# Optimization experiments

Hardware: AMD Instinct MI355X
Metric: run time of the kernel (lower is better)

Reference implementation:

```python
import jax, jax.numpy as jnp
import numpy as np

HIDDEN = 256

def setup_inputs() -> dict:
    key = jax.random.key(0)
    ks = jax.random.split(key, 7)
    B, S, H = 4, 4096, HIDDEN
    x = jax.random.normal(ks[0], (B, S, H), dtype=jnp.float32)
    s = 1.0 / np.sqrt(H)
    Wq = jax.random.normal(ks[1], (H, H), dtype=jnp.float32) * s
    bq = jax.random.normal(ks[2], (H,), dtype=jnp.float32) * s
    Wk = jax.random.normal(ks[3], (H, H), dtype=jnp.float32) * s
    bk = jax.random.normal(ks[4], (H,), dtype=jnp.float32) * s
    Wv = jax.random.normal(ks[5], (H, H), dtype=jnp.float32) * s
    bv = jax.random.normal(ks[6], (H,), dtype=jnp.float32) * s
    return {"x": x, "Wq": Wq, "bq": bq, "Wk": Wk, "bk": bk, "Wv": Wv, "bv": bv}

def reference(x, Wq, bq, Wk, bk, Wv, bv):
    # Linear projections (torch Linear: x @ W.T + b; here W stored as [in,out])
    Q = x @ Wq + bq  # [B,S,H]
    K = x @ Wk + bk
    V = x @ Wv + bv
    S = x.shape[1]
    # NOTE: original module has NO 1/sqrt(d) scaling — kept faithful.
    scores = jnp.einsum('bqh,bkh->bqk', Q, K)  # [B,S,S]
    causal = jnp.tril(jnp.ones((S, S), dtype=bool))
    scores = jnp.where(causal, scores, -jnp.inf)
    attn = jax.nn.softmax(scores, axis=-1)
    return jnp.einsum('bqk,bkh->bqh', attn, V)
```

## Files before the change

### kernel.cpp

```cpp
#include <hip/hip_runtime.h>
#include <stdint.h>

#define HD   256
#define SEQ  4096
#define NB   4
#define NROW (NB * SEQ)
#define SLOTS_PER_BATCH 144

typedef __attribute__((ext_vector_type(8))) short short8;
typedef __attribute__((ext_vector_type(4))) float f32x4;
typedef __attribute__((ext_vector_type(16))) float f32x16;
typedef _Float16 v8h __attribute__((ext_vector_type(8)));

__device__ __forceinline__ unsigned short f2bf(float f) {
  union { float f; unsigned u; } v; v.f = f;
  unsigned u = v.u;
  u += 0x7fffu + ((u >> 16) & 1u);
  return (unsigned short)(u >> 16);
}
__device__ __forceinline__ float bf2f(unsigned short h) {
  union { float f; unsigned u; } v; v.u = ((unsigned)h) << 16;
  return v.f;
}
__device__ __forceinline__ unsigned short f2h(float f) {
  union { _Float16 h; unsigned short u; } v;
  v.h = (_Float16)f;
  return v.u;
}

__device__ __forceinline__ f32x4 mfma16(short8 a, short8 b, f32x4 c) {
  return __builtin_amdgcn_mfma_f32_16x16x32_bf16(a, b, c, 0, 0, 0);
}
__device__ __forceinline__ f32x16 mfma32h(v8h a, v8h b, f32x16 c) {
  return __builtin_amdgcn_mfma_f32_32x32x16_f16(a, b, c, 0, 0, 0);
}

__device__ __forceinline__ void gload_lds16(const void* g, void* l) {
  __builtin_amdgcn_global_load_lds((const __attribute__((address_space(1))) void*)g,
                                   (__attribute__((address_space(3))) void*)l,
                                   16, 0, 0);
}

__device__ __forceinline__ unsigned pk2h(float a, float b) {
  return (unsigned)f2h(a) | ((unsigned)f2h(b) << 16);
}

__global__ __launch_bounds__(256) void prep_x_kernel(
    const float* __restrict__ x,
    unsigned short* __restrict__ xh, unsigned short* __restrict__ xl)
{
  int i = blockIdx.x * 256 + threadIdx.x;
  const float* p = x + i * 8;
  f32x4 a0 = *(const f32x4*)p;
  f32x4 a1 = *(const f32x4*)(p + 4);
  short8 hh, ll;
#pragma unroll
  for (int j = 0; j < 4; ++j) {
    unsigned short h0 = f2bf(a0[j]);
    hh[j]     = (short)h0;
    ll[j]     = (short)f2bf(a0[j] - bf2f(h0));
    unsigned short h1 = f2bf(a1[j]);
    hh[4 + j] = (short)h1;
    ll[4 + j] = (short)f2bf(a1[j] - bf2f(h1));
  }
  *(short8*)(xh + i * 8) = hh;
  *(short8*)(xl + i * 8) = ll;
}

__global__ __launch_bounds__(256) void prep_w_kernel(
    const float* __restrict__ Wq, const float* __restrict__ Wk,
    const float* __restrict__ Wv,
    unsigned short* __restrict__ WTh, unsigned short* __restrict__ WTl)
{
  int flat = blockIdx.x * 256 + threadIdx.x;
  int mat = flat >> 16;
  int e   = flat & 65535;
  int o   = e >> 8;
  int k   = e & 255;
  const float* W = (mat == 0) ? Wq : (mat == 1) ? Wk : Wv;
  float v = W[k * 256 + o];
  unsigned short h = f2bf(v);
  WTh[flat] = h;
  WTl[flat] = f2bf(v - bf2f(h));
}

__global__ __launch_bounds__(256) void proj_kernel(
    const unsigned short* __restrict__ xh, const unsigned short* __restrict__ xl,
    const unsigned short* __restrict__ WTh, const unsigned short* __restrict__ WTl,
    const float* __restrict__ bq, const float* __restrict__ bk,
    const float* __restrict__ bv,
    unsigned short* __restrict__ Qf, unsigned short* __restrict__ Kf,
    unsigned short* __restrict__ VT)
{
  const int mat = blockIdx.y;
  const int r0  = blockIdx.x << 6;
  const int tid = threadIdx.x;
  const int w    = tid >> 6;
  const int lane = tid & 63;
  const int lr   = lane & 15;
  const int hi4  = lane >> 4;
  const int r4   = hi4 << 2;

  const unsigned short* wth = WTh + (mat << 16);
  const unsigned short* wtl = WTl + (mat << 16);

  f32x4 acc[4][4] = {};

#pragma unroll
  for (int ks = 0; ks < 8; ++ks) {
    short8 ah[4], al[4];
#pragma unroll
    for (int m = 0; m < 4; ++m) {
      int off = (r0 + (m << 4) + lr) * 256 + (ks << 5) + (hi4 << 3);
      ah[m] = *(const short8*)(xh + off);
      al[m] = *(const short8*)(xl + off);
    }
#pragma unroll
    for (int n = 0; n < 4; ++n) {
      int o = (w << 6) + (n << 4) + lr;
      short8 bh = *(const short8*)(wth + o * 256 + (ks << 5) + (hi4 << 3));
      short8 bl = *(const short8*)(wtl + o * 256 + (ks << 5) + (hi4 << 3));
#pragma unroll
      for (int m = 0; m < 4; ++m) acc[m][n] = mfma16(ah[m], bh, acc[m][n]);
#pragma unroll
      for (int m = 0; m < 4; ++m) acc[m][n] = mfma16(al[m], bh, acc[m][n]);
#pragma unroll
      for (int m = 0; m < 4; ++m) acc[m][n] = mfma16(ah[m], bl, acc[m][n]);
    }
  }

  const float* bias = (mat == 0) ? bq : (mat == 1) ? bk : bv;
#pragma unroll
  for (int n = 0; n < 4; ++n) {
    int col = (w << 6) + (n << 4) + lr;
    float bb = bias[col];
#pragma unroll
    for (int m = 0; m < 4; ++m) {
#pragma unroll
      for (int reg = 0; reg < 4; ++reg) {
        int row = r0 + (m << 4) + r4 + reg;
        float val = acc[m][n][reg] + bb;
        unsigned short h = f2h(val);
        if (mat == 0) {
          Qf[row * 256 + col] = h;
        } else if (mat == 1) {
          Kf[row * 256 + col] = h;
        } else {
          int b = row >> 12, s = row & 4095;
          VT[(b << 20) + (col << 12) + s] = h;
        }
      }
    }
  }
}

__global__ __launch_bounds__(256, 2) void attn_kernel(
    const unsigned short* __restrict__ Qf, const unsigned short* __restrict__ Kf,
    const unsigned short* __restrict__ VT,
    unsigned short* __restrict__ Opart, float* __restrict__ Mpart,
    float* __restrict__ Lpart)
{
  __shared__ __align__(16) unsigned short sK[64 * 256];
  __shared__ __align__(16) unsigned short sV[256 * 64];

  const int bx    = blockIdx.x;
  const int batch = bx & 3;
  const int rk    = bx >> 2;
  int j = 0, pj = 0;
  while (rk >= pj + ((j + 4) >> 2)) { pj += (j + 4) >> 2; ++j; }
  const int c   = rk - pj;
  const int kt0 = c << 3;
  const int kt1 = min(kt0 + 8, 2 * j + 2);
  const int slot = batch * SLOTS_PER_BATCH + pj + c;

  const int tid  = threadIdx.x;
  const int w    = tid >> 6;
  const int lane = tid & 63;
  const int lc   = lane & 31;
  const int hi   = lane >> 5;

  const unsigned short* Kf_b = Kf + (batch << 20);
  const unsigned short* VT_b = VT + (batch << 20);

  auto stage = [&](int kt) {
#pragma unroll
    for (int it = 0; it < 8; ++it) {
      int id = it * 256 + tid;
      int kr = id >> 5, cb = id & 31;
      gload_lds16(Kf_b + (((kt << 6) + kr) << 8) + (((cb ^ kr) & 31) << 3),
                  sK + id * 8);
      int hd = id >> 3, cb2 = id & 7;
      gload_lds16(VT_b + (hd << 12) + (kt << 6) + (((cb2 ^ (hd >> 2)) & 7) << 3),
                  sV + id * 8);
    }
  };

  f32x16 oacc[8];
  float m_ = -1e30f, accl = 0.f;
#pragma unroll
  for (int n = 0; n < 8; ++n)
#pragma unroll
    for (int r = 0; r < 16; ++r) oacc[n][r] = 0.f;

  for (int kt = kt0; kt < kt1; ++kt) {
    stage(kt);
    __syncthreads();

    int qrow = (batch << 12) + (j << 7) + (w << 5) + lc;
    uintptr_t qv = (uintptr_t)Qf + ((size_t)qrow << 9) + (hi << 4);
    asm volatile("" : "+v"(qv));
    const unsigned short* qp = (const unsigned short*)qv;

    f32x16 s0, s1;
#pragma unroll
    for (int r = 0; r < 16; ++r) { s0[r] = 0.f; s1[r] = 0.f; }
    __builtin_amdgcn_s_setprio(1);
#pragma unroll
    for (int ks = 0; ks < 16; ++ks) {
      int cc = (ks << 1) + hi;
      v8h qa  = *(const v8h*)(qp + (ks << 4));
      v8h kb0 = *(const v8h*)(sK + (lc << 8) + (((cc ^ lc) & 31) << 3));
      v8h kb1 = *(const v8h*)(sK + ((32 + lc) << 8) + (((cc ^ lc) & 31) << 3));
      s0 = mfma32h(kb0, qa, s0);
      s1 = mfma32h(kb1, qa, s1);
    }
    __builtin_amdgcn_s_setprio(0);

    const int qg = (j << 7) + (w << 5) + lc;
    if ((kt << 6) + 63 > (j << 7) + (w << 5)) {
#pragma unroll
      for (int r = 0; r < 16; ++r) {
        int kl = (kt << 6) + (r & 3) + ((r >> 2) << 3) + (hi << 2);
        if (kl > qg)      s0[r] = -3e38f;
        if (kl + 32 > qg) s1[r] = -3e38f;
      }
    }

    float mx = fmaxf(s0[0], s1[0]);
#pragma unroll
    for (int r = 1; r < 16; ++r) mx = fmaxf(mx, fmaxf(s0[r], s1[r]));
    mx = fmaxf(mx, __shfl_xor(mx, 32));

    if (__any(mx > m_ + 8.0f)) {
      float mn = fmaxf(m_, mx);
      float sc = __expf(m_ - mn);
      m_ = mn;
      accl *= sc;
#pragma unroll
      for (int r = 0; r < 16; ++r) {
        float scr = __shfl(sc, (r & 3) + ((r >> 2) << 3) + (hi << 2));
#pragma unroll
        for (int n = 0; n < 8; ++n) oacc[n][r] *= scr;
      }
    }

#pragma unroll
    for (int r = 0; r < 16; ++r) {
      s0[r] = __expf(s0[r] - m_);
      s1[r] = __expf(s1[r] - m_);
      accl += s0[r] + s1[r];
    }

    v8h pa[4];
#pragma unroll
    for (int half = 0; half < 2; ++half) {
      const f32x16& ps = half ? s1 : s0;
#pragma unroll
      for (int t2 = 0; t2 < 2; ++t2) {
        int b = t2 << 3;
        unsigned X0 = pk2h(ps[b + 0], ps[b + 1]);
        unsigned X1 = pk2h(ps[b + 2], ps[b + 3]);
        unsigned Y0 = pk2h(ps[b + 4], ps[b + 5]);
        unsigned Y1 = pk2h(ps[b + 6], ps[b + 7]);
        unsigned xs0 = (unsigned)__shfl_xor((int)X0, 32);
        unsigned xs1 = (unsigned)__shfl_xor((int)X1, 32);
        unsigned ys0 = (unsigned)__shfl_xor((int)Y0, 32);
        unsigned ys1 = (unsigned)__shfl_xor((int)Y1, 32);
        union { unsigned u[4]; v8h h; } pu;
        pu.u[0] = hi ? ys0 : X0;
        pu.u[1] = hi ? ys1 : X1;
        pu.u[2] = hi ? Y0 : xs0;
        pu.u[3] = hi ? Y1 : xs1;
        pa[(half << 1) + t2] = pu.h;
      }
    }

    __builtin_amdgcn_s_setprio(1);
#pragma unroll
    for (int ks2 = 0; ks2 < 4; ++ks2) {
      int cc = (ks2 << 1) + hi;
#pragma unroll
      for (int n = 0; n < 8; ++n) {
        int hd = (n << 5) + lc;
        v8h vb = *(const v8h*)(sV + (hd << 6) + (((cc ^ (hd >> 2)) & 7) << 3));
        oacc[n] = mfma32h(pa[ks2], vb, oacc[n]);
      }
    }
    __builtin_amdgcn_s_setprio(0);

    __syncthreads();
  }

  {
    unsigned short* Op = Opart + (size_t)slot * (128 * 256);
    float lt  = accl + __shfl_xor(accl, 32);
    float inv = (lt > 0.f) ? (1.0f / lt) : 0.f;
#pragma unroll
    for (int n = 0; n < 8; ++n) {
#pragma unroll
      for (int r = 0; r < 16; ++r) {
        int crow = (r & 3) + ((r >> 2) << 3) + (hi << 2);
        float invr = __shfl(inv, crow);
        Op[((w << 5) + crow) * 256 + (n << 5) + lc] = f2h(oacc[n][r] * invr);
      }
    }
    if (lane < 32) {
      Mpart[slot * 128 + (w << 5) + lc] = m_;
      Lpart[slot * 128 + (w << 5) + lc] = lt;
    }
  }
}

__global__ __launch_bounds__(256) void merge_kernel(
    const unsigned short* __restrict__ Opart, const float* __restrict__ Mpart,
    const float* __restrict__ Lpart, float* __restrict__ out)
{
  int t = blockIdx.x * 256 + threadIdx.x;
  int row = t >> 5, c8 = t & 31;
  int batch = row >> 12, wi = row & 4095;
  int j = wi >> 7, rloc = wi & 127;
  int q  = j >> 2;
  int pj = 2 * q * (q + 1) + (j - 4 * q) * (q + 1);
  int nch = (j + 4) >> 2;
  int sbase = batch * SLOTS_PER_BATCH + pj;

  float M = -1e30f;
  for (int i = 0; i < nch; ++i)
    M = fmaxf(M, Mpart[(sbase + i) * 128 + rloc]);

  float denom = 0.f;
  float r8[8] = {0.f, 0.f, 0.f, 0.f, 0.f, 0.f, 0.f, 0.f};
  for (int i = 0; i < nch; ++i) {
    float mi = Mpart[(sbase + i) * 128 + rloc];
    float li = Lpart[(sbase + i) * 128 + rloc];
    float wgt = __expf(mi - M) * li;
    denom += wgt;
    const unsigned short* Op =
        Opart + ((size_t)(sbase + i) * 128 + rloc) * 256 + (c8 << 3);
    v8h v = *(const v8h*)Op;
#pragma unroll
    for (int qq = 0; qq < 8; ++qq) r8[qq] += wgt * (float)v[qq];
  }
  float inv = 1.0f / denom;
  float* op = out + (size_t)row * 256 + (c8 << 3);
  f32x4 r0, r1;
#pragma unroll
  for (int qq = 0; qq < 4; ++qq) { r0[qq] = r8[qq] * inv; r1[qq] = r8[4 + qq] * inv; }
  *(f32x4*)op = r0;
  *(f32x4*)(op + 4) = r1;
}

extern "C" void kernel_launch(void* const* d_in, const int* in_sizes, int n_in,
                              void* d_out, int out_size, void* d_ws, size_t ws_size,
                              hipStream_t stream) {
  (void)in_sizes; (void)n_in; (void)out_size; (void)ws_size;
  const float* x  = (const float*)d_in[0];
  const float* Wq = (const float*)d_in[1];
  const float* bq = (const float*)d_in[2];
  const float* Wk = (const float*)d_in[3];
  const float* bk = (const float*)d_in[4];
  const float* Wv = (const float*)d_in[5];
  const float* bv = (const float*)d_in[6];
  float* out = (float*)d_out;

  const int nslots = NB * SLOTS_PER_BATCH;
  unsigned short* Qf = (unsigned short*)d_ws;
  unsigned short* Kf = Qf + (size_t)NROW * HD;
  unsigned short* VT = Kf + (size_t)NROW * HD;
  float* Mpart = (float*)(VT + (size_t)NROW * HD);
  float* Lpart = Mpart + (size_t)nslots * 128;
  unsigned short* regionBase = (unsigned short*)(Lpart + (size_t)nslots * 128);
  unsigned short* xh  = regionBase;
  unsigned short* xl  = xh + (size_t)NROW * HD;
  unsigned short* WTh = xl + (size_t)NROW * HD;
  unsigned short* WTl = WTh + 3 * 65536;
  unsigned short* Opart = regionBase;

  hipLaunchKernelGGL(prep_x_kernel, dim3(2048), dim3(256), 0, stream,
                     x, xh, xl);
  hipLaunchKernelGGL(prep_w_kernel, dim3(768), dim3(256), 0, stream,
                     Wq, Wk, Wv, WTh, WTl);
  hipLaunchKernelGGL(proj_kernel, dim3(256, 3), dim3(256), 0, stream,
                     xh, xl, WTh, WTl, bq, bk, bv, Qf, Kf, VT);
  hipLaunchKernelGGL(attn_kernel, dim3(NB * SLOTS_PER_BATCH), dim3(256), 0, stream,
                     Qf, Kf, VT, Opart, Mpart, Lpart);
  hipLaunchKernelGGL(merge_kernel, dim3(2048), dim3(256), 0, stream,
                     Opart, Mpart, Lpart, out);
}
```

Baseline: 233.7 us.

## Fuse x bf16 split into projection and double-buffer 32-key attention tiles

Removes the separate prep_x kernel and its xh/xl workspace by converting fp32 x to hi/lo bf16 inside the projection kernel's operand loads. The attention kernel now uses 32-key tiles with two LDS buffers, issuing the next tile's global-to-LDS loads before computing the current one and waiting with vmcnt plus raw barriers instead of syncthreads. This aims to hide K/V load latency and save a kernel launch plus an x round trip. In exchange there are more loop iterations with smaller MFMA batches, more softmax rescale checks, and the conversion is recomputed three times (once per projection matrix).

```diff
diff --git a/kernel.cpp b/kernel.cpp
--- a/kernel.cpp
+++ b/kernel.cpp
@@ -43,28 +43,6 @@
 
 __device__ __forceinline__ unsigned pk2h(float a, float b) {
   return (unsigned)f2h(a) | ((unsigned)f2h(b) << 16);
-}
-
-__global__ __launch_bounds__(256) void prep_x_kernel(
-    const float* __restrict__ x,
-    unsigned short* __restrict__ xh, unsigned short* __restrict__ xl)
-{
-  int i = blockIdx.x * 256 + threadIdx.x;
-  const float* p = x + i * 8;
-  f32x4 a0 = *(const f32x4*)p;
-  f32x4 a1 = *(const f32x4*)(p + 4);
-  short8 hh, ll;
-#pragma unroll
-  for (int j = 0; j < 4; ++j) {
-    unsigned short h0 = f2bf(a0[j]);
-    hh[j]     = (short)h0;
-    ll[j]     = (short)f2bf(a0[j] - bf2f(h0));
-    unsigned short h1 = f2bf(a1[j]);
-    hh[4 + j] = (short)h1;
-    ll[4 + j] = (short)f2bf(a1[j] - bf2f(h1));
-  }
-  *(short8*)(xh + i * 8) = hh;
-  *(short8*)(xl + i * 8) = ll;
 }
 
 __global__ __launch_bounds__(256) void prep_w_kernel(
@@ -85,7 +63,7 @@
 }
 
 __global__ __launch_bounds__(256) void proj_kernel(
-    const unsigned short* __restrict__ xh, const unsigned short* __restrict__ xl,
+    const float* __restrict__ x,
     const unsigned short* __restrict__ WTh, const unsigned short* __restrict__ WTl,
     const float* __restrict__ bq, const float* __restrict__ bk,
     const float* __restrict__ bv,
@@ -111,9 +89,20 @@
     short8 ah[4], al[4];
 #pragma unroll
     for (int m = 0; m < 4; ++m) {
-      int off = (r0 + (m << 4) + lr) * 256 + (ks << 5) + (hi4 << 3);
-      ah[m] = *(const short8*)(xh + off);
-      al[m] = *(const short8*)(xl + off);
+      const float* xp = x + (r0 + (m << 4) + lr) * 256 + (ks << 5) + (hi4 << 3);
+      f32x4 a0 = *(const f32x4*)xp;
+      f32x4 a1 = *(const f32x4*)(xp + 4);
+      short8 hh, ll;
+#pragma unroll
+      for (int jj = 0; jj < 4; ++jj) {
+        unsigned short h0 = f2bf(a0[jj]);
+        hh[jj]     = (short)h0;
+        ll[jj]     = (short)f2bf(a0[jj] - bf2f(h0));
+        unsigned short h1 = f2bf(a1[jj]);
+        hh[4 + jj] = (short)h1;
+        ll[4 + jj] = (short)f2bf(a1[jj] - bf2f(h1));
+      }
+      ah[m] = hh; al[m] = ll;
     }
 #pragma unroll
     for (int n = 0; n < 4; ++n) {
@@ -160,8 +149,8 @@
     unsigned short* __restrict__ Opart, float* __restrict__ Mpart,
     float* __restrict__ Lpart)
 {
-  __shared__ __align__(16) unsigned short sK[64 * 256];
-  __shared__ __align__(16) unsigned short sV[256 * 64];
+  __shared__ __align__(16) unsigned short sK[2][32 * 256];
+  __shared__ __align__(16) unsigned short sV[2][256 * 32];
 
   const int bx    = blockIdx.x;
   const int batch = bx & 3;
@@ -169,8 +158,8 @@
   int j = 0, pj = 0;
   while (rk >= pj + ((j + 4) >> 2)) { pj += (j + 4) >> 2; ++j; }
   const int c   = rk - pj;
-  const int kt0 = c << 3;
-  const int kt1 = min(kt0 + 8, 2 * j + 2);
+  const int kt0 = c << 4;
+  const int kt1 = min(kt0 + 16, 4 * j + 4);
   const int slot = batch * SLOTS_PER_BATCH + pj + c;
 
   const int tid  = threadIdx.x;
@@ -182,16 +171,16 @@
   const unsigned short* Kf_b = Kf + (batch << 20);
   const unsigned short* VT_b = VT + (batch << 20);
 
-  auto stage = [&](int kt) {
-#pragma unroll
-    for (int it = 0; it < 8; ++it) {
+  auto stage = [&](int kt, int buf) {
+#pragma unroll
+    for (int it = 0; it < 4; ++it) {
       int id = it * 256 + tid;
       int kr = id >> 5, cb = id & 31;
-      gload_lds16(Kf_b + (((kt << 6) + kr) << 8) + (((cb ^ kr) & 31) << 3),
-                  sK + id * 8);
-      int hd = id >> 3, cb2 = id & 7;
-      gload_lds16(VT_b + (hd << 12) + (kt << 6) + (((cb2 ^ (hd >> 2)) & 7) << 3),
-                  sV + id * 8);
+      gload_lds16(Kf_b + (((kt << 5) + kr) << 8) + (((cb ^ kr) & 31) << 3),
+                  &sK[buf][id * 8]);
+      int hd = id >> 2, cb2 = id & 3;
+      gload_lds16(VT_b + (hd << 12) + (kt << 5) + (((cb2 ^ (hd >> 2)) & 3) << 3),
+                  &sV[buf][id * 8]);
     }
   };
 
@@ -202,43 +191,50 @@
 #pragma unroll
     for (int r = 0; r < 16; ++r) oacc[n][r] = 0.f;
 
+  const int qg = (j << 7) + (w << 5) + lc;
+
+  stage(kt0, 0);
+  int cur = 0;
+
   for (int kt = kt0; kt < kt1; ++kt) {
-    stage(kt);
-    __syncthreads();
-
-    int qrow = (batch << 12) + (j << 7) + (w << 5) + lc;
+    const bool havenext = (kt + 1 < kt1);
+    if (havenext) stage(kt + 1, cur ^ 1);
+    __builtin_amdgcn_sched_barrier(0);
+    if (havenext) { asm volatile("s_waitcnt vmcnt(8)" ::: "memory"); }
+    else          { asm volatile("s_waitcnt vmcnt(0)" ::: "memory"); }
+    __builtin_amdgcn_sched_barrier(0);
+    __builtin_amdgcn_s_barrier();
+    __builtin_amdgcn_sched_barrier(0);
+
+    int qrow = (batch << 12) + qg;
     uintptr_t qv = (uintptr_t)Qf + ((size_t)qrow << 9) + (hi << 4);
     asm volatile("" : "+v"(qv));
     const unsigned short* qp = (const unsigned short*)qv;
 
-    f32x16 s0, s1;
-#pragma unroll
-    for (int r = 0; r < 16; ++r) { s0[r] = 0.f; s1[r] = 0.f; }
+    f32x16 s0;
+#pragma unroll
+    for (int r = 0; r < 16; ++r) s0[r] = 0.f;
     __builtin_amdgcn_s_setprio(1);
 #pragma unroll
     for (int ks = 0; ks < 16; ++ks) {
       int cc = (ks << 1) + hi;
       v8h qa  = *(const v8h*)(qp + (ks << 4));
-      v8h kb0 = *(const v8h*)(sK + (lc << 8) + (((cc ^ lc) & 31) << 3));
-      v8h kb1 = *(const v8h*)(sK + ((32 + lc) << 8) + (((cc ^ lc) & 31) << 3));
+      v8h kb0 = *(const v8h*)(&sK[cur][(lc << 8) + (((cc ^ lc) & 31) << 3)]);
       s0 = mfma32h(kb0, qa, s0);
-      s1 = mfma32h(kb1, qa, s1);
     }
     __builtin_amdgcn_s_setprio(0);
 
-    const int qg = (j << 7) + (w << 5) + lc;
-    if ((kt << 6) + 63 > (j << 7) + (w << 5)) {
+    if ((kt << 5) + 31 > (j << 7) + (w << 5)) {
 #pragma unroll
       for (int r = 0; r < 16; ++r) {
-        int kl = (kt << 6) + (r & 3) + ((r >> 2) << 3) + (hi << 2);
-        if (kl > qg)      s0[r] = -3e38f;
-        if (kl + 32 > qg) s1[r] = -3e38f;
-      }
-    }
-
-    float mx = fmaxf(s0[0], s1[0]);
-#pragma unroll
-    for (int r = 1; r < 16; ++r) mx = fmaxf(mx, fmaxf(s0[r], s1[r]));
+        int kl = (kt << 5) + (r & 3) + ((r >> 2) << 3) + (hi << 2);
+        if (kl > qg) s0[r] = -3e38f;
+      }
+    }
+
+    float mx = s0[0];
+#pragma unroll
+    for (int r = 1; r < 16; ++r) mx = fmaxf(mx, s0[r]);
     mx = fmaxf(mx, __shfl_xor(mx, 32));
 
     if (__any(mx > m_ + 8.0f)) {
@@ -257,48 +253,46 @@
 #pragma unroll
     for (int r = 0; r < 16; ++r) {
       s0[r] = __expf(s0[r] - m_);
-      s1[r] = __expf(s1[r] - m_);
-      accl += s0[r] + s1[r];
-    }
-
-    v8h pa[4];
-#pragma unroll
-    for (int half = 0; half < 2; ++half) {
-      const f32x16& ps = half ? s1 : s0;
-#pragma unroll
-      for (int t2 = 0; t2 < 2; ++t2) {
-        int b = t2 << 3;
-        unsigned X0 = pk2h(ps[b + 0], ps[b + 1]);
-        unsigned X1 = pk2h(ps[b + 2], ps[b + 3]);
-        unsigned Y0 = pk2h(ps[b + 4], ps[b + 5]);
-        unsigned Y1 = pk2h(ps[b + 6], ps[b + 7]);
-        unsigned xs0 = (unsigned)__shfl_xor((int)X0, 32);
-        unsigned xs1 = (unsigned)__shfl_xor((int)X1, 32);
-        unsigned ys0 = (unsigned)__shfl_xor((int)Y0, 32);
-        unsigned ys1 = (unsigned)__shfl_xor((int)Y1, 32);
-        union { unsigned u[4]; v8h h; } pu;
-        pu.u[0] = hi ? ys0 : X0;
-        pu.u[1] = hi ? ys1 : X1;
-        pu.u[2] = hi ? Y0 : xs0;
-        pu.u[3] = hi ? Y1 : xs1;
-        pa[(half << 1) + t2] = pu.h;
-      }
+      accl += s0[r];
+    }
+
+    v8h pa[2];
+#pragma unroll
+    for (int t2 = 0; t2 < 2; ++t2) {
+      int b = t2 << 3;
+      unsigned X0 = pk2h(s0[b + 0], s0[b + 1]);
+      unsigned X1 = pk2h(s0[b + 2], s0[b + 3]);
+      unsigned Y0 = pk2h(s0[b + 4], s0[b + 5]);
+      unsigned Y1 = pk2h(s0[b + 6], s0[b + 7]);
+      unsigned xs0 = (unsigned)__shfl_xor((int)X0, 32);
+      unsigned xs1 = (unsigned)__shfl_xor((int)X1, 32);
+      unsigned ys0 = (unsigned)__shfl_xor((int)Y0, 32);
+      unsigned ys1 = (unsigned)__shfl_xor((int)Y1, 32);
+      union { unsigned u[4]; v8h h; } pu;
+      pu.u[0] = hi ? ys0 : X0;
+      pu.u[1] = hi ? ys1 : X1;
+      pu.u[2] = hi ? Y0 : xs0;
+      pu.u[3] = hi ? Y1 : xs1;
+      pa[t2] = pu.h;
     }
 
     __builtin_amdgcn_s_setprio(1);
 #pragma unroll
-    for (int ks2 = 0; ks2 < 4; ++ks2) {
+    for (int ks2 = 0; ks2 < 2; ++ks2) {
       int cc = (ks2 << 1) + hi;
 #pragma unroll
       for (int n = 0; n < 8; ++n) {
         int hd = (n << 5) + lc;
-        v8h vb = *(const v8h*)(sV + (hd << 6) + (((cc ^ (hd >> 2)) & 7) << 3));
+        v8h vb = *(const v8h*)(&sV[cur][(hd << 5) + (((cc ^ (hd >> 2)) & 3) << 3)]);
         oacc[n] = mfma32h(pa[ks2], vb, oacc[n]);
       }
     }
     __builtin_amdgcn_s_setprio(0);
 
-    __syncthreads();
+    __builtin_amdgcn_sched_barrier(0);
+    __builtin_amdgcn_s_barrier();
+    __builtin_amdgcn_sched_barrier(0);
+    cur ^= 1;
   }
 
   {
@@ -380,18 +374,14 @@
   float* Mpart = (float*)(VT + (size_t)NROW * HD);
   float* Lpart = Mpart + (size_t)nslots * 128;
   unsigned short* regionBase = (unsigned short*)(Lpart + (size_t)nslots * 128);
-  unsigned short* xh  = regionBase;
-  unsigned short* xl  = xh + (size_t)NROW * HD;
-  unsigned short* WTh = xl + (size_t)NROW * HD;
+  unsigned short* WTh = regionBase;
   unsigned short* WTl = WTh + 3 * 65536;
   unsigned short* Opart = regionBase;
 
-  hipLaunchKernelGGL(prep_x_kernel, dim3(2048), dim3(256), 0, stream,
-                     x, xh, xl);
   hipLaunchKernelGGL(prep_w_kernel, dim3(768), dim3(256), 0, stream,
                      Wq, Wk, Wv, WTh, WTl);
   hipLaunchKernelGGL(proj_kernel, dim3(256, 3), dim3(256), 0, stream,
-                     xh, xl, WTh, WTl, bq, bk, bv, Qf, Kf, VT);
+                     x, WTh, WTl, bq, bk, bv, Qf, Kf, VT);
   hipLaunchKernelGGL(attn_kernel, dim3(NB * SLOTS_PER_BATCH), dim3(256), 0, stream,
                      Qf, Kf, VT, Opart, Mpart, Lpart);
   hipLaunchKernelGGL(merge_kernel, dim3(2048), dim3(256), 0, stream,
```

New measurement: 268.7 us. 15.0% more time.
